# Kernel tuning notes

Hardware: AMD Instinct MI355X
Metric: run time of the kernel (lower is better)

Reference implementation:

```python
import math
import jax, jax.numpy as jnp
import numpy as np

HEAD = 16
D_STATE = 12
DT_RANK = 1


def _ln(x, w, b, eps):
    mu = jnp.mean(x, axis=-1, keepdims=True)
    xc = x - mu
    var = jnp.mean(xc * xc, axis=-1, keepdims=True)
    return xc * jax.lax.rsqrt(var + eps) * w + b


def _chan_ln(x, w, b, eps=1e-6):
    # LayerNorm over channel axis of (B, C, H, W)
    return _ln(x.transpose(0, 2, 3, 1), w, b, eps).transpose(0, 3, 1, 2)


def _gconv1x1(x, w):
    # grouped 1x1 conv; x: (B, Cin, H, W), w: (G, Cout_per_g, Cin_per_g)
    B, Cin, H, W = x.shape
    G, Co, Ci = w.shape
    xg = x.reshape(B, G, Ci, H, W)
    y = jnp.einsum('bgihw,goi->bgohw', xg, w)
    return y.reshape(B, G * Co, H, W)


def _dwconv(x, w, b):
    # depthwise 3x3 conv, SAME padding; w: (C, 1, 3, 3)
    y = jax.lax.conv_general_dilated(x, w, (1, 1), 'SAME',
                                     feature_group_count=x.shape[1])
    return y + b[None, :, None, None]


def setup_inputs() -> dict:
    key = jax.random.key(0)
    ks = jax.random.split(key, 16)
    B, C, H, W = 2, 96, 128, 128
    G, E = 24, 192           # groups = C//4, expand_d = 2*C
    c = E // HEAD            # d_inner per head = 12
    R, N = DT_RANK, D_STATE
    f32 = jnp.float32
    inp = {}
    inp['x_rgb'] = jax.random.normal(ks[0], (B, C, H, W), f32)
    inp['x_e'] = jax.random.normal(ks[1], (B, C, H, W), f32)
    inp['in1_w'] = jnp.ones((C,), f32); inp['in1_b'] = jnp.zeros((C,), f32)
    inp['in2_w'] = jnp.ones((C,), f32); inp['in2_b'] = jnp.zeros((C,), f32)
    inp['inproj_rgb_w'] = jax.random.normal(ks[2], (G, E // G, C // G), f32) * 0.2
    inp['inproj_e_w'] = jax.random.normal(ks[3], (G, E // G, C // G), f32) * 0.2
    inp['conv_rgb_w'] = jax.random.normal(ks[4], (E, 1, 3, 3), f32) * 0.2
    inp['conv_rgb_b'] = jnp.zeros((E,), f32)
    inp['conv_e_w'] = jax.random.normal(ks[5], (E, 1, 3, 3), f32) * 0.2
    inp['conv_e_b'] = jnp.zeros((E,), f32)
    inp['xproj_w'] = jax.random.normal(ks[6], (2, R + 2 * N, HEAD), f32) * (HEAD ** -0.5)
    inp['dtproj_w'] = jax.random.uniform(ks[7], (2, HEAD, R), f32, -R ** -0.5, R ** -0.5)
    dt = jnp.exp(jax.random.uniform(ks[8], (2, HEAD), f32)
                 * (math.log(0.1) - math.log(0.001)) + math.log(0.001))
    dt = jnp.clip(dt, 1e-4, None)
    inp['dtproj_b'] = dt + jnp.log(-jnp.expm1(-dt))  # inverse softplus
    inp['A_logs'] = jnp.log(jnp.broadcast_to(jnp.arange(1, N + 1, dtype=f32), (2, HEAD, N)))
    inp['Ds'] = jnp.ones((2, HEAD), f32)
    inp['on1_w'] = jnp.ones((c,), f32); inp['on1_b'] = jnp.zeros((c,), f32)
    inp['on2_w'] = jnp.ones((c,), f32); inp['on2_b'] = jnp.zeros((c,), f32)
    inp['outproj_rgb_w'] = jax.random.normal(ks[9], (G, C // G, E // G), f32) * 0.2
    inp['outproj_e_w'] = jax.random.normal(ks[10], (G, C // G, E // G), f32) * 0.2
    inp['n1_w'] = jnp.ones((C,), f32); inp['n1_b'] = jnp.zeros((C,), f32)
    inp['n2_w'] = jnp.ones((C,), f32); inp['n2_b'] = jnp.zeros((C,), f32)
    Hd = 4 * C
    inp['mlp_rgb_fc1_w'] = jax.random.normal(ks[11], (Hd, C), f32) * 0.1
    inp['mlp_rgb_fc1_b'] = jnp.zeros((Hd,), f32)
    inp['mlp_rgb_fc2_w'] = jax.random.normal(ks[12], (C, Hd), f32) * 0.05
    inp['mlp_rgb_fc2_b'] = jnp.zeros((C,), f32)
    inp['mlp_e_fc1_w'] = jax.random.normal(ks[13], (Hd, C), f32) * 0.1
    inp['mlp_e_fc1_b'] = jnp.zeros((Hd,), f32)
    inp['mlp_e_fc2_w'] = jax.random.normal(ks[14], (C, Hd), f32) * 0.05
    inp['mlp_e_fc2_b'] = jnp.zeros((C,), f32)
    return inp


def reference(x_rgb, x_e, in1_w, in1_b, in2_w, in2_b, inproj_rgb_w, inproj_e_w,
              conv_rgb_w, conv_rgb_b, conv_e_w, conv_e_b, xproj_w, dtproj_w,
              dtproj_b, A_logs, Ds, on1_w, on1_b, on2_w, on2_b,
              outproj_rgb_w, outproj_e_w, n1_w, n1_b, n2_w, n2_b,
              mlp_rgb_fc1_w, mlp_rgb_fc1_b, mlp_rgb_fc2_w, mlp_rgb_fc2_b,
              mlp_e_fc1_w, mlp_e_fc1_b, mlp_e_fc2_w, mlp_e_fc2_b):
    B, C, H, W = x_rgb.shape
    L = H * W
    R, N = DT_RANK, D_STATE
    # input layer norms (eps=1e-6) over channels
    xr = _chan_ln(x_rgb, in1_w, in1_b)
    xe = _chan_ln(x_e, in2_w, in2_b)
    # grouped 1x1 expand + depthwise conv + SiLU
    ur = jax.nn.silu(_dwconv(_gconv1x1(xr, inproj_rgb_w), conv_rgb_w, conv_rgb_b))
    ue = jax.nn.silu(_dwconv(_gconv1x1(xe, inproj_e_w), conv_e_w, conv_e_b))
    c = ur.shape[1] // HEAD  # d_inner per head

    def to_head(x):  # (B, E, H, W) -> (B, L, head, c)
        return x.transpose(0, 2, 3, 1).reshape(B, L, HEAD, c)

    xs = jnp.stack([to_head(ur), to_head(ue)], axis=2)  # (B, L, 2, head, c)
    # input-dependent dt, B, C projections from the per-head feature (dim=head)
    x_dbl = jnp.einsum('blkdc,krd->blkrc', xs, xproj_w)
    dts = x_dbl[..., :R, :]
    Bs = x_dbl[..., R:R + N, :]          # (B, L, 2, N, c)
    Cs = x_dbl[..., R + N:, :]
    dt = jnp.einsum('blkrc,kdr->blkdc', dts, dtproj_w) + dtproj_b[None, None, :, :, None]
    dt = jax.nn.softplus(dt)             # (B, L, 2, head, c)
    A = -jnp.exp(A_logs)                 # (2, head, N)
    Cs_cross = Cs[:, :, ::-1]            # cross-modal readout: swap modalities
    # selective scan over the channel dim c (sequence axis)
    dt_t = jnp.moveaxis(dt, -1, 0)
    u_t = jnp.moveaxis(xs, -1, 0)
    B_t = jnp.moveaxis(Bs, -1, 0)
    C_t = jnp.moveaxis(Cs_cross, -1, 0)
    h0 = jnp.zeros((B, L, 2, HEAD, N), xs.dtype)

    def step(h, inps):
        dt_s, u_s, B_s, C_s = inps
        dA = jnp.exp(dt_s[..., None] * A)                       # (B,L,2,head,N)
        h = dA * h + (dt_s * u_s)[..., None] * B_s[:, :, :, None, :]
        y = jnp.einsum('blkdn,blkn->blkd', h, C_s)
        return h, y

    _, ys = jax.lax.scan(step, h0, (dt_t, u_t, B_t, C_t))
    y = jnp.moveaxis(ys, 0, -1) + xs * Ds[None, None, :, :, None]  # (B,L,2,head,c)
    # per-head LayerNorm over c (eps=1e-5), back to (B, E, H, W)
    y_r = _ln(y[:, :, 0], on1_w, on1_b, 1e-5).reshape(B, H, W, HEAD * c).transpose(0, 3, 1, 2)
    y_e = _ln(y[:, :, 1], on2_w, on2_b, 1e-5).reshape(B, H, W, HEAD * c).transpose(0, 3, 1, 2)
    y_r = _gconv1x1(y_r, outproj_rgb_w) + xr
    y_e = _gconv1x1(y_e, outproj_e_w) + xe

    def mlp(x, nw, nb, w1, b1, w2, b2):
        z = _chan_ln(x, nw, nb)
        z = jnp.einsum('bchw,oc->bohw', z, w1) + b1[None, :, None, None]
        z = jax.nn.gelu(z, approximate=False)
        z = jnp.einsum('bohw,co->bchw', z, w2) + b2[None, :, None, None]
        return x + z

    y_r = mlp(y_r, n1_w, n1_b, mlp_rgb_fc1_w, mlp_rgb_fc1_b, mlp_rgb_fc2_w, mlp_rgb_fc2_b)
    y_e = mlp(y_e, n2_w, n2_b, mlp_e_fc1_w, mlp_e_fc1_b, mlp_e_fc2_w, mlp_e_fc2_b)
    return (y_r, y_e)
```

## Files before the change

kernel.cpp:

```cpp
#include <hip/hip_runtime.h>
#include <math.h>

#define HWn 16384
#define Hn  128
#define Wn  128
#define Bn  2
#define Cn  96
#define En  192
#define Gn  24
#define HEADn 16
#define CCn 12
#define Nn  12
#define HDn 384

__global__ __launch_bounds__(256) void k_ln_inproj(
    const float* __restrict__ x0, const float* __restrict__ x1,
    const float* __restrict__ lw0, const float* __restrict__ lb0,
    const float* __restrict__ lw1, const float* __restrict__ lb1,
    const float* __restrict__ pw0, const float* __restrict__ pw1,
    float* __restrict__ xr, float* __restrict__ v)
{
  const int s  = blockIdx.y;
  const int gp = blockIdx.x * 256 + threadIdx.x;
  const int b  = gp >> 14, l = gp & (HWn - 1);
  const float* x  = s ? x1  : x0;
  const float* lw = s ? lw1 : lw0;
  const float* lb = s ? lb1 : lb0;
  const float* pw = s ? pw1 : pw0;

  float xv[Cn];
  float sum = 0.f, ss = 0.f;
  const float* xp = x + (size_t)b * Cn * HWn + l;
#pragma unroll
  for (int ch = 0; ch < Cn; ++ch) {
    float t = xp[(size_t)ch * HWn];
    xv[ch] = t; sum += t; ss += t * t;
  }
  float mu  = sum * (1.f / Cn);
  float var = ss * (1.f / Cn) - mu * mu;
  float rs  = rsqrtf(var + 1e-6f);

  float* xrp = xr + ((size_t)s * Bn + b) * Cn * HWn + l;
#pragma unroll
  for (int ch = 0; ch < Cn; ++ch) {
    float n = fmaf((xv[ch] - mu) * rs, lw[ch], lb[ch]);
    xv[ch] = n;
    xrp[(size_t)ch * HWn] = n;
  }

  float* vp = v + ((size_t)s * Bn + b) * En * HWn + l;
#pragma unroll
  for (int g = 0; g < Gn; ++g) {
#pragma unroll
    for (int o = 0; o < 8; ++o) {
      float a = 0.f;
#pragma unroll
      for (int i = 0; i < 4; ++i) a = fmaf(xv[g * 4 + i], pw[g * 32 + o * 4 + i], a);
      vp[(size_t)(g * 8 + o) * HWn] = a;
    }
  }
}

__global__ __launch_bounds__(256) void k_dwconv_silu(
    const float* __restrict__ v,
    const float* __restrict__ cw0, const float* __restrict__ cb0,
    const float* __restrict__ cw1, const float* __restrict__ cb1,
    float* __restrict__ u)
{
  const int z = blockIdx.z;
  const int e = blockIdx.y;
  const int p = blockIdx.x * 256 + threadIdx.x;
  const int h = p >> 7, w = p & 127;
  const int s = z >> 1;
  const float* cw  = (s ? cw1 : cw0) + e * 9;
  const float bias = (s ? cb1 : cb0)[e];
  const float* src = v + ((size_t)z * En + e) * HWn;

  float acc = bias;
#pragma unroll
  for (int kh = 0; kh < 3; ++kh) {
    int hh = h + kh - 1;
    if (hh < 0 || hh >= Hn) continue;
#pragma unroll
    for (int kw = 0; kw < 3; ++kw) {
      int ww = w + kw - 1;
      if (ww < 0 || ww >= Wn) continue;
      acc = fmaf(src[hh * Wn + ww], cw[kh * 3 + kw], acc);
    }
  }
  float sig = 1.f / (1.f + expf(-acc));
  u[((size_t)z * En + e) * HWn + p] = acc * sig;
}

#define UPXS 417
#define USS  208
#define UDS  13
#define XPXS 604
#define XSS  300

__global__ __launch_bounds__(512) void k_ssm(
    const float* __restrict__ u_ws, const float* __restrict__ xr_ws,
    float* __restrict__ z_ws,
    const float* __restrict__ xprojw, const float* __restrict__ dtprojw,
    const float* __restrict__ dtprojb, const float* __restrict__ A_logs,
    const float* __restrict__ Ds,
    const float* __restrict__ on1w, const float* __restrict__ on1b,
    const float* __restrict__ on2w, const float* __restrict__ on2b,
    const float* __restrict__ opw0, const float* __restrict__ opw1)
{
  __shared__ __align__(16) float uS[16 * UPXS];
  __shared__ __align__(16) float xdl[16 * XPXS];

  const int tid  = threadIdx.x;
  const int tile = blockIdx.x;
  const int b  = (tile * 16) >> 14;
  const int l0 = (tile * 16) & (HWn - 1);

  const int p2px = tid >> 5, p2s = (tid >> 4) & 1, p2d = tid & 15;
  const float dtw = dtprojw[p2s * HEADn + p2d];
  const float dtb = dtprojb[p2s * HEADn + p2d];
  const float Dv  = Ds[p2s * HEADn + p2d];
  float Ar[Nn];
  {
    const float4* ap = (const float4*)&A_logs[(p2s * HEADn + p2d) * Nn];
    float4 a0 = ap[0], a1 = ap[1], a2 = ap[2];
    Ar[0]=-expf(a0.x); Ar[1]=-expf(a0.y); Ar[2]=-expf(a0.z); Ar[3]=-expf(a0.w);
    Ar[4]=-expf(a1.x); Ar[5]=-expf(a1.y); Ar[6]=-expf(a1.z); Ar[7]=-expf(a1.w);
    Ar[8]=-expf(a2.x); Ar[9]=-expf(a2.y); Ar[10]=-expf(a2.z); Ar[11]=-expf(a2.w);
  }

#pragma unroll
  for (int i = 0; i < 3; ++i) {
    int id = i * 512 + tid;
    int px4 = id & 3, rest = id >> 2;
    int ch = rest % En, s2 = rest / En;
    float4 t = *(const float4*)&u_ws[(((size_t)s2 * Bn + b) * En + ch) * HWn + l0 + px4 * 4];
    int dd = ch / 12, cc = ch % 12;
    int base = s2 * USS + dd * UDS + cc;
    uS[(px4 * 4 + 0) * UPXS + base] = t.x;
    uS[(px4 * 4 + 1) * UPXS + base] = t.y;
    uS[(px4 * 4 + 2) * UPXS + base] = t.z;
    uS[(px4 * 4 + 3) * UPXS + base] = t.w;
  }
  __syncthreads();

#pragma unroll
  for (int j = 0; j < 2; ++j) {
    int id = j * 512 + tid;
    if (id < 800) {
      int px = id & 15, sr = id >> 4;
      int s2 = sr / 25, r = sr % 25;
      const float4* xw4 = (const float4*)&xprojw[(s2 * 25 + r) * HEADn];
      float4 w0 = xw4[0], w1 = xw4[1], w2 = xw4[2], w3 = xw4[3];
      float wv[16];
      wv[0]=w0.x; wv[1]=w0.y; wv[2]=w0.z; wv[3]=w0.w;
      wv[4]=w1.x; wv[5]=w1.y; wv[6]=w1.z; wv[7]=w1.w;
      wv[8]=w2.x; wv[9]=w2.y; wv[10]=w2.z; wv[11]=w2.w;
      wv[12]=w3.x; wv[13]=w3.y; wv[14]=w3.z; wv[15]=w3.w;
      int ub = px * UPXS + s2 * USS;
      float acc[12];
#pragma unroll
      for (int cc = 0; cc < 12; ++cc) acc[cc] = 0.f;
#pragma unroll
      for (int dd = 0; dd < HEADn; ++dd) {
        float w = wv[dd];
        int ua = ub + dd * UDS;
#pragma unroll
        for (int cc = 0; cc < 12; ++cc)
          acc[cc] = fmaf(uS[ua + cc], w, acc[cc]);
      }
      float* xp = &xdl[px * XPXS + s2 * XSS + r * 12];
      *(float4*)&xp[0] = make_float4(acc[0], acc[1], acc[2], acc[3]);
      *(float4*)&xp[4] = make_float4(acc[4], acc[5], acc[6], acc[7]);
      *(float4*)&xp[8] = make_float4(acc[8], acc[9], acc[10], acc[11]);
    }
  }
  __syncthreads();

  {
    const int px = p2px, s = p2s, d = p2d;
    const int ub = px * UPXS + s * USS + d * UDS;
    float uvv[12];
#pragma unroll
    for (int cc = 0; cc < 12; ++cc) uvv[cc] = uS[ub + cc];

    const int xb = px * XPXS;
    float dts[12];
    {
      const float4* dr = (const float4*)&xdl[xb + s * XSS];
      float4 q0 = dr[0], q1 = dr[1], q2 = dr[2];
      dts[0]=q0.x; dts[1]=q0.y; dts[2]=q0.z; dts[3]=q0.w;
      dts[4]=q1.x; dts[5]=q1.y; dts[6]=q1.z; dts[7]=q1.w;
      dts[8]=q2.x; dts[9]=q2.y; dts[10]=q2.z; dts[11]=q2.w;
    }
    float dt_s[12], dtu[12];
#pragma unroll
    for (int cc = 0; cc < 12; ++cc) {
      float pre = fmaf(dts[cc], dtw, dtb);
      float v = (pre > 20.f) ? pre : log1pf(expf(pre));
      dt_s[cc] = v;
      dtu[cc] = v * uvv[cc];
    }

    float y[12];
#pragma unroll
    for (int cc = 0; cc < 12; ++cc) y[cc] = 0.f;

#pragma unroll
    for (int n = 0; n < Nn; ++n) {
      const float4* Br = (const float4*)&xdl[xb + s * XSS + (1 + n) * 12];
      const float4* Cr = (const float4*)&xdl[xb + (1 - s) * XSS + (13 + n) * 12];
      float4 b0 = Br[0], b1 = Br[1], b2 = Br[2];
      float4 c0 = Cr[0], c1 = Cr[1], c2 = Cr[2];
      float Bv[12], Cv[12];
      Bv[0]=b0.x; Bv[1]=b0.y; Bv[2]=b0.z; Bv[3]=b0.w;
      Bv[4]=b1.x; Bv[5]=b1.y; Bv[6]=b1.z; Bv[7]=b1.w;
      Bv[8]=b2.x; Bv[9]=b2.y; Bv[10]=b2.z; Bv[11]=b2.w;
      Cv[0]=c0.x; Cv[1]=c0.y; Cv[2]=c0.z; Cv[3]=c0.w;
      Cv[4]=c1.x; Cv[5]=c1.y; Cv[6]=c1.z; Cv[7]=c1.w;
      Cv[8]=c2.x; Cv[9]=c2.y; Cv[10]=c2.z; Cv[11]=c2.w;
      float h = 0.f;
      float An = Ar[n];
#pragma unroll
      for (int cc = 0; cc < 12; ++cc) {
        float dA = expf(dt_s[cc] * An);
        h = fmaf(dA, h, dtu[cc] * Bv[cc]);
        y[cc] = fmaf(h, Cv[cc], y[cc]);
      }
    }

#pragma unroll
    for (int cc = 0; cc < 12; ++cc) y[cc] = fmaf(uvv[cc], Dv, y[cc]);

    float mu = 0.f;
#pragma unroll
    for (int cc = 0; cc < 12; ++cc) mu += y[cc];
    mu *= (1.f / CCn);
    float var = 0.f;
#pragma unroll
    for (int cc = 0; cc < 12; ++cc) { float t = y[cc] - mu; var = fmaf(t, t, var); }
    var *= (1.f / CCn);
    float rs = rsqrtf(var + 1e-5f);
    const float* ow = s ? on2w : on1w;
    const float* ob = s ? on2b : on1b;
#pragma unroll
    for (int cc = 0; cc < 12; ++cc)
      uS[ub + cc] = fmaf((y[cc] - mu) * rs, ow[cc], ob[cc]);
  }
  __syncthreads();

#pragma unroll
  for (int i = 0; i < 2; ++i) {
    int id = i * 512 + tid;
    if (id < 768) {
      int px4 = id & 3, ch = (id >> 2) % Cn, ss = id / 384;
      int g = ch >> 2, co = ch & 3;
      const float* ow2 = (ss ? opw1 : opw0) + g * 32 + co * 8;
      float a0 = 0.f, a1 = 0.f, a2 = 0.f, a3 = 0.f;
#pragma unroll
      for (int ci = 0; ci < 8; ++ci) {
        int e = g * 8 + ci;
        int dd = e / 12, cc = e % 12;
        int base = ss * USS + dd * UDS + cc;
        float w = ow2[ci];
        a0 = fmaf(uS[(px4 * 4 + 0) * UPXS + base], w, a0);
        a1 = fmaf(uS[(px4 * 4 + 1) * UPXS + base], w, a1);
        a2 = fmaf(uS[(px4 * 4 + 2) * UPXS + base], w, a2);
        a3 = fmaf(uS[(px4 * 4 + 3) * UPXS + base], w, a3);
      }
      size_t go = (((size_t)ss * Bn + b) * Cn + ch) * HWn + l0 + px4 * 4;
      float4 xrv = *(const float4*)&xr_ws[go];
      *(float4*)&z_ws[go] =
          make_float4(a0 + xrv.x, a1 + xrv.y, a2 + xrv.z, a3 + xrv.w);
    }
  }
}

__global__ void k_transpose_w(
    const float* __restrict__ w1r, const float* __restrict__ w1e,
    const float* __restrict__ w2r, const float* __restrict__ w2e,
    float* __restrict__ w1t, float* __restrict__ w2t)
{
  int idx = blockIdx.x * 256 + threadIdx.x;
  int which = idx / 36864;
  int r = idx % 36864;
  if (which < 2) {
    int c = r / HDn, o = r % HDn;
    const float* src = which ? w1e : w1r;
    w1t[which * 36864 + r] = src[o * Cn + c];
  } else {
    int o = r / Cn, c = r % Cn;
    const float* src = (which == 3) ? w2e : w2r;
    w2t[(which - 2) * 36864 + r] = src[c * HDn + o];
  }
}

__global__ __launch_bounds__(256, 2) void k_mlp(
    const float* __restrict__ z_all,
    const float* __restrict__ n1w, const float* __restrict__ n1b,
    const float* __restrict__ n2w, const float* __restrict__ n2b,
    const float* __restrict__ w1t_all, const float* __restrict__ b1r,
    const float* __restrict__ b1e,
    const float* __restrict__ w2t_all, const float* __restrict__ b2r,
    const float* __restrict__ b2e,
    float* __restrict__ out_all)
{
  __shared__ float zn[Cn * 32];
  __shared__ float hS[HDn * 32];
  __shared__ float red[2 * 8 * 32];
  __shared__ float mus[32], rss[32];

  const int s    = blockIdx.y;
  const int tile = blockIdx.x;
  const int b    = (tile * 32) >> 14;
  const int l0   = (tile * 32) & (HWn - 1);
  const int tid  = threadIdx.x;

  const float* z   = z_all + ((size_t)s * Bn + b) * Cn * HWn + l0;
  float*       out = (float*)out_all + ((size_t)s * Bn + b) * Cn * HWn + l0;
  const float* nw  = s ? n2w : n1w;
  const float* nb  = s ? n2b : n1b;
  const float* w1t = w1t_all + s * 36864;
  const float* b1  = s ? b1e : b1r;
  const float* w2t = w2t_all + s * 36864;
  const float* b2  = s ? b2e : b2r;

  {
    const int px = tid & 31, part = tid >> 5;
    float psum = 0.f, pss = 0.f;
#pragma unroll
    for (int i = 0; i < 12; ++i) {
      int c = part + 8 * i;
      float v = z[(size_t)c * HWn + px];
      zn[c * 32 + px] = v; psum += v; pss += v * v;
    }
    red[part * 32 + px] = psum;
    red[256 + part * 32 + px] = pss;
    __syncthreads();
    if (tid < 32) {
      float sm = 0.f, sq = 0.f;
#pragma unroll
      for (int p = 0; p < 8; ++p) { sm += red[p * 32 + tid]; sq += red[256 + p * 32 + tid]; }
      float mu = sm * (1.f / Cn);
      float var = sq * (1.f / Cn) - mu * mu;
      mus[tid] = mu; rss[tid] = rsqrtf(var + 1e-6f);
    }
    __syncthreads();
    float mu = mus[px], rs = rss[px];
#pragma unroll
    for (int i = 0; i < 12; ++i) {
      int c = part + 8 * i;
      float v = zn[c * 32 + px];
      zn[c * 32 + px] = fmaf((v - mu) * rs, nw[c], nb[c]);
    }
    __syncthreads();
  }

  const int pg = (tid & 7) << 2;

  {
    const int og = (tid >> 3) * 12;
    float acc[12][4];
#pragma unroll
    for (int j = 0; j < 12; ++j)
#pragma unroll
      for (int i = 0; i < 4; ++i) acc[j][i] = 0.f;

    for (int c = 0; c < Cn; ++c) {
      const float* zr = &zn[c * 32 + pg];
      float x0 = zr[0], x1 = zr[1], x2 = zr[2], x3 = zr[3];
      const float* wr = &w1t[c * HDn + og];
#pragma unroll
      for (int j = 0; j < 12; ++j) {
        float w = wr[j];
        acc[j][0] = fmaf(x0, w, acc[j][0]);
        acc[j][1] = fmaf(x1, w, acc[j][1]);
        acc[j][2] = fmaf(x2, w, acc[j][2]);
        acc[j][3] = fmaf(x3, w, acc[j][3]);
      }
    }
#pragma unroll
    for (int j = 0; j < 12; ++j) {
      float bo = b1[og + j];
      float* hr = &hS[(og + j) * 32 + pg];
#pragma unroll
      for (int i = 0; i < 4; ++i) {
        float a = acc[j][i] + bo;
        hr[i] = 0.5f * a * (1.f + erff(a * 0.70710678118654752f));
      }
    }
  }
  __syncthreads();

  {
    const int cg = (tid >> 3) * 3;
    float a0[4], a1[4], a2[4];
#pragma unroll
    for (int i = 0; i < 4; ++i) { a0[i] = 0.f; a1[i] = 0.f; a2[i] = 0.f; }

    for (int o = 0; o < HDn; ++o) {
      const float* hr = &hS[o * 32 + pg];
      float x0 = hr[0], x1 = hr[1], x2 = hr[2], x3 = hr[3];
      const float* wr = &w2t[o * Cn + cg];
      float w0 = wr[0], w1 = wr[1], w2 = wr[2];
      a0[0] = fmaf(x0, w0, a0[0]); a0[1] = fmaf(x1, w0, a0[1]);
      a0[2] = fmaf(x2, w0, a0[2]); a0[3] = fmaf(x3, w0, a0[3]);
      a1[0] = fmaf(x0, w1, a1[0]); a1[1] = fmaf(x1, w1, a1[1]);
      a1[2] = fmaf(x2, w1, a1[2]); a1[3] = fmaf(x3, w1, a1[3]);
      a2[0] = fmaf(x0, w2, a2[0]); a2[1] = fmaf(x1, w2, a2[1]);
      a2[2] = fmaf(x2, w2, a2[2]); a2[3] = fmaf(x3, w2, a2[3]);
    }
#pragma unroll
    for (int k = 0; k < 3; ++k) {
      int c = cg + k;
      float bk = b2[c];
      const float* ak = (k == 0) ? a0 : (k == 1) ? a1 : a2;
#pragma unroll
      for (int i = 0; i < 4; ++i) {
        size_t off = (size_t)c * HWn + pg + i;
        out[off] = ak[i] + bk + z[off];
      }
    }
  }
}

extern "C" void kernel_launch(void* const* d_in, const int* in_sizes, int n_in,
                              void* d_out, int out_size, void* d_ws, size_t ws_size,
                              hipStream_t stream)
{
  const float* x_rgb = (const float*)d_in[0];
  const float* x_e   = (const float*)d_in[1];
  const float* in1_w = (const float*)d_in[2];
  const float* in1_b = (const float*)d_in[3];
  const float* in2_w = (const float*)d_in[4];
  const float* in2_b = (const float*)d_in[5];
  const float* ipw0  = (const float*)d_in[6];
  const float* ipw1  = (const float*)d_in[7];
  const float* cw0   = (const float*)d_in[8];
  const float* cb0   = (const float*)d_in[9];
  const float* cw1   = (const float*)d_in[10];
  const float* cb1   = (const float*)d_in[11];
  const float* xprojw  = (const float*)d_in[12];
  const float* dtprojw = (const float*)d_in[13];
  const float* dtprojb = (const float*)d_in[14];
  const float* A_logs  = (const float*)d_in[15];
  const float* Ds      = (const float*)d_in[16];
  const float* on1w  = (const float*)d_in[17];
  const float* on1b  = (const float*)d_in[18];
  const float* on2w  = (const float*)d_in[19];
  const float* on2b  = (const float*)d_in[20];
  const float* opw0  = (const float*)d_in[21];
  const float* opw1  = (const float*)d_in[22];
  const float* n1w   = (const float*)d_in[23];
  const float* n1b   = (const float*)d_in[24];
  const float* n2w   = (const float*)d_in[25];
  const float* n2b   = (const float*)d_in[26];
  const float* w1r   = (const float*)d_in[27];
  const float* b1r   = (const float*)d_in[28];
  const float* w2r   = (const float*)d_in[29];
  const float* b2r   = (const float*)d_in[30];
  const float* w1e   = (const float*)d_in[31];
  const float* b1e   = (const float*)d_in[32];
  const float* w2e   = (const float*)d_in[33];
  const float* b2e   = (const float*)d_in[34];

  float* ws  = (float*)d_ws;
  float* xr  = ws;
  float* vz  = ws + (size_t)6291456;
  float* ut  = ws + (size_t)18874368;
  float* w1t = ut;
  float* w2t = ut + 73728;

  dim3 b256(256);

  k_ln_inproj<<<dim3(128, 2), b256, 0, stream>>>(
      x_rgb, x_e, in1_w, in1_b, in2_w, in2_b, ipw0, ipw1, xr, vz);

  k_dwconv_silu<<<dim3(64, En, 4), b256, 0, stream>>>(
      vz, cw0, cb0, cw1, cb1, ut);

  k_ssm<<<dim3(2048), dim3(512), 0, stream>>>(
      ut, xr, vz, xprojw, dtprojw, dtprojb, A_logs, Ds,
      on1w, on1b, on2w, on2b, opw0, opw1);

  k_transpose_w<<<dim3(576), b256, 0, stream>>>(w1r, w1e, w2r, w2e, w1t, w2t);

  k_mlp<<<dim3(1024, 2), b256, 0, stream>>>(
      vz, n1w, n1b, n2w, n2b, w1t, b1r, b1e, w2t, b2r, b2e, (float*)d_out);
}
```

Before: 585.9 us.

## Tile LN+in-projection through shared memory and split MLP hidden dim in halves

k_ln_inproj now processes 64-pixel tiles per block, staging the input in shared memory with float4 loads. A block-level reduction computes the LayerNorm statistics, and the grouped projection runs from LDS, replacing one thread per pixel holding 96 registers. The grid grows from 256 to 1024 blocks, which should raise occupancy. k_mlp splits the 384-wide hidden layer into two 192 halves so the hidden-activation shared buffer halves, letting 4 blocks per CU fit, and widens loads to float2/float4 with fewer accumulators per thread. The extra syncs and repeated fc2 accumulation passes add some overhead.

```diff
diff --git a/kernel.cpp b/kernel.cpp
--- a/kernel.cpp
+++ b/kernel.cpp
@@ -13,51 +13,94 @@
 #define Nn  12
 #define HDn 384
 
-__global__ __launch_bounds__(256) void k_ln_inproj(
+#define ZS 68
+
+__global__ __launch_bounds__(256, 4) void k_ln_inproj(
     const float* __restrict__ x0, const float* __restrict__ x1,
     const float* __restrict__ lw0, const float* __restrict__ lb0,
     const float* __restrict__ lw1, const float* __restrict__ lb1,
     const float* __restrict__ pw0, const float* __restrict__ pw1,
     float* __restrict__ xr, float* __restrict__ v)
 {
-  const int s  = blockIdx.y;
-  const int gp = blockIdx.x * 256 + threadIdx.x;
-  const int b  = gp >> 14, l = gp & (HWn - 1);
+  __shared__ __align__(16) float zn[Cn * ZS];
+  __shared__ float red[2 * 16 * 64];
+  __shared__ float mus[64], rss[64];
+
+  const int s    = blockIdx.y;
+  const int tile = blockIdx.x;
+  const int b  = (tile * 64) >> 14;
+  const int l0 = (tile * 64) & (HWn - 1);
+  const int tid = threadIdx.x;
+
   const float* x  = s ? x1  : x0;
   const float* lw = s ? lw1 : lw0;
   const float* lb = s ? lb1 : lb0;
   const float* pw = s ? pw1 : pw0;
 
-  float xv[Cn];
-  float sum = 0.f, ss = 0.f;
-  const float* xp = x + (size_t)b * Cn * HWn + l;
-#pragma unroll
-  for (int ch = 0; ch < Cn; ++ch) {
-    float t = xp[(size_t)ch * HWn];
-    xv[ch] = t; sum += t; ss += t * t;
-  }
-  float mu  = sum * (1.f / Cn);
-  float var = ss * (1.f / Cn) - mu * mu;
-  float rs  = rsqrtf(var + 1e-6f);
-
-  float* xrp = xr + ((size_t)s * Bn + b) * Cn * HWn + l;
-#pragma unroll
-  for (int ch = 0; ch < Cn; ++ch) {
-    float n = fmaf((xv[ch] - mu) * rs, lw[ch], lb[ch]);
-    xv[ch] = n;
-    xrp[(size_t)ch * HWn] = n;
-  }
-
-  float* vp = v + ((size_t)s * Bn + b) * En * HWn + l;
-#pragma unroll
-  for (int g = 0; g < Gn; ++g) {
-#pragma unroll
-    for (int o = 0; o < 8; ++o) {
-      float a = 0.f;
-#pragma unroll
-      for (int i = 0; i < 4; ++i) a = fmaf(xv[g * 4 + i], pw[g * 32 + o * 4 + i], a);
-      vp[(size_t)(g * 8 + o) * HWn] = a;
-    }
+  const int px4 = (tid & 15) * 4;
+  const int cg0 = tid >> 4;
+
+  const float* xp = x + (size_t)b * Cn * HWn + l0;
+  float ps0=0.f,ps1=0.f,ps2=0.f,ps3=0.f, pq0=0.f,pq1=0.f,pq2=0.f,pq3=0.f;
+#pragma unroll
+  for (int i = 0; i < 6; ++i) {
+    int ch = cg0 + 16 * i;
+    float4 t = *(const float4*)&xp[(size_t)ch * HWn + px4];
+    *(float4*)&zn[ch * ZS + px4] = t;
+    ps0 += t.x; pq0 += t.x * t.x;
+    ps1 += t.y; pq1 += t.y * t.y;
+    ps2 += t.z; pq2 += t.z * t.z;
+    ps3 += t.w; pq3 += t.w * t.w;
+  }
+  red[cg0 * 64 + px4 + 0] = ps0; red[1024 + cg0 * 64 + px4 + 0] = pq0;
+  red[cg0 * 64 + px4 + 1] = ps1; red[1024 + cg0 * 64 + px4 + 1] = pq1;
+  red[cg0 * 64 + px4 + 2] = ps2; red[1024 + cg0 * 64 + px4 + 2] = pq2;
+  red[cg0 * 64 + px4 + 3] = ps3; red[1024 + cg0 * 64 + px4 + 3] = pq3;
+  __syncthreads();
+  if (tid < 64) {
+    float sm = 0.f, sq = 0.f;
+#pragma unroll
+    for (int g = 0; g < 16; ++g) { sm += red[g * 64 + tid]; sq += red[1024 + g * 64 + tid]; }
+    float mu = sm * (1.f / Cn);
+    float var = sq * (1.f / Cn) - mu * mu;
+    mus[tid] = mu; rss[tid] = rsqrtf(var + 1e-6f);
+  }
+  __syncthreads();
+
+  const float m0 = mus[px4+0], m1 = mus[px4+1], m2 = mus[px4+2], m3 = mus[px4+3];
+  const float r0 = rss[px4+0], r1 = rss[px4+1], r2 = rss[px4+2], r3 = rss[px4+3];
+  float* xrp = xr + ((size_t)s * Bn + b) * Cn * HWn + l0;
+#pragma unroll
+  for (int i = 0; i < 6; ++i) {
+    int ch = cg0 + 16 * i;
+    float4 t = *(const float4*)&zn[ch * ZS + px4];
+    float wch = lw[ch], bch = lb[ch];
+    t.x = fmaf((t.x - m0) * r0, wch, bch);
+    t.y = fmaf((t.y - m1) * r1, wch, bch);
+    t.z = fmaf((t.z - m2) * r2, wch, bch);
+    t.w = fmaf((t.w - m3) * r3, wch, bch);
+    *(float4*)&zn[ch * ZS + px4] = t;
+    *(float4*)&xrp[(size_t)ch * HWn + px4] = t;
+  }
+  __syncthreads();
+
+  const int og  = (tid >> 4) * 12;
+  const int pxg = (tid & 15) * 4;
+  float* vp = v + ((size_t)s * Bn + b) * En * HWn + l0;
+#pragma unroll
+  for (int jo = 0; jo < 12; ++jo) {
+    int o = og + jo, g = o >> 3;
+    float4 wv = *(const float4*)&pw[g * 32 + (o & 7) * 4];
+    float4 z0 = *(const float4*)&zn[(g * 4 + 0) * ZS + pxg];
+    float4 z1 = *(const float4*)&zn[(g * 4 + 1) * ZS + pxg];
+    float4 z2 = *(const float4*)&zn[(g * 4 + 2) * ZS + pxg];
+    float4 z3 = *(const float4*)&zn[(g * 4 + 3) * ZS + pxg];
+    float4 a;
+    a.x = fmaf(z0.x, wv.x, fmaf(z1.x, wv.y, fmaf(z2.x, wv.z, z3.x * wv.w)));
+    a.y = fmaf(z0.y, wv.x, fmaf(z1.y, wv.y, fmaf(z2.y, wv.z, z3.y * wv.w)));
+    a.z = fmaf(z0.z, wv.x, fmaf(z1.z, wv.y, fmaf(z2.z, wv.z, z3.z * wv.w)));
+    a.w = fmaf(z0.w, wv.x, fmaf(z1.w, wv.y, fmaf(z2.w, wv.z, z3.w * wv.w)));
+    *(float4*)&vp[(size_t)o * HWn + pxg] = a;
   }
 }
 
@@ -295,7 +338,9 @@
   }
 }
 
-__global__ __launch_bounds__(256, 2) void k_mlp(
+#define HSS 34
+
+__global__ __launch_bounds__(256, 4) void k_mlp(
     const float* __restrict__ z_all,
     const float* __restrict__ n1w, const float* __restrict__ n1b,
     const float* __restrict__ n2w, const float* __restrict__ n2b,
@@ -306,7 +351,7 @@
     float* __restrict__ out_all)
 {
   __shared__ float zn[Cn * 32];
-  __shared__ float hS[HDn * 32];
+  __shared__ float hS[192 * HSS];
   __shared__ float red[2 * 8 * 32];
   __shared__ float mus[32], rss[32];
 
@@ -356,71 +401,78 @@
     __syncthreads();
   }
 
-  const int pg = (tid & 7) << 2;
-
-  {
-    const int og = (tid >> 3) * 12;
-    float acc[12][4];
-#pragma unroll
-    for (int j = 0; j < 12; ++j)
+  const int pg   = (tid & 7) << 2;
+  const int og   = (tid >> 3) * 6;
+  const int p2px = (tid & 15) * 2;
+  const int cg   = (tid >> 4) * 6;
+
+  float a2[6][2];
+#pragma unroll
+  for (int k = 0; k < 6; ++k) { a2[k][0] = 0.f; a2[k][1] = 0.f; }
+
+#pragma unroll
+  for (int hf = 0; hf < 2; ++hf) {
+    float acc[6][4];
+#pragma unroll
+    for (int j = 0; j < 6; ++j)
 #pragma unroll
       for (int i = 0; i < 4; ++i) acc[j][i] = 0.f;
 
+    const float* w1base = w1t + hf * 192 + og;
     for (int c = 0; c < Cn; ++c) {
-      const float* zr = &zn[c * 32 + pg];
-      float x0 = zr[0], x1 = zr[1], x2 = zr[2], x3 = zr[3];
-      const float* wr = &w1t[c * HDn + og];
-#pragma unroll
-      for (int j = 0; j < 12; ++j) {
-        float w = wr[j];
-        acc[j][0] = fmaf(x0, w, acc[j][0]);
-        acc[j][1] = fmaf(x1, w, acc[j][1]);
-        acc[j][2] = fmaf(x2, w, acc[j][2]);
-        acc[j][3] = fmaf(x3, w, acc[j][3]);
+      float4 xv = *(const float4*)&zn[c * 32 + pg];
+      const float* wr = w1base + c * HDn;
+      float2 wa = *(const float2*)&wr[0];
+      float2 wb = *(const float2*)&wr[2];
+      float2 wc = *(const float2*)&wr[4];
+      float w[6] = {wa.x, wa.y, wb.x, wb.y, wc.x, wc.y};
+#pragma unroll
+      for (int j = 0; j < 6; ++j) {
+        acc[j][0] = fmaf(xv.x, w[j], acc[j][0]);
+        acc[j][1] = fmaf(xv.y, w[j], acc[j][1]);
+        acc[j][2] = fmaf(xv.z, w[j], acc[j][2]);
+        acc[j][3] = fmaf(xv.w, w[j], acc[j][3]);
       }
     }
 #pragma unroll
-    for (int j = 0; j < 12; ++j) {
-      float bo = b1[og + j];
-      float* hr = &hS[(og + j) * 32 + pg];
-#pragma unroll
-      for (int i = 0; i < 4; ++i) {
-        float a = acc[j][i] + bo;
-        hr[i] = 0.5f * a * (1.f + erff(a * 0.70710678118654752f));
-      }
-    }
-  }
-  __syncthreads();
-
-  {
-    const int cg = (tid >> 3) * 3;
-    float a0[4], a1[4], a2[4];
-#pragma unroll
-    for (int i = 0; i < 4; ++i) { a0[i] = 0.f; a1[i] = 0.f; a2[i] = 0.f; }
-
-    for (int o = 0; o < HDn; ++o) {
-      const float* hr = &hS[o * 32 + pg];
-      float x0 = hr[0], x1 = hr[1], x2 = hr[2], x3 = hr[3];
-      const float* wr = &w2t[o * Cn + cg];
-      float w0 = wr[0], w1 = wr[1], w2 = wr[2];
-      a0[0] = fmaf(x0, w0, a0[0]); a0[1] = fmaf(x1, w0, a0[1]);
-      a0[2] = fmaf(x2, w0, a0[2]); a0[3] = fmaf(x3, w0, a0[3]);
-      a1[0] = fmaf(x0, w1, a1[0]); a1[1] = fmaf(x1, w1, a1[1]);
-      a1[2] = fmaf(x2, w1, a1[2]); a1[3] = fmaf(x3, w1, a1[3]);
-      a2[0] = fmaf(x0, w2, a2[0]); a2[1] = fmaf(x1, w2, a2[1]);
-      a2[2] = fmaf(x2, w2, a2[2]); a2[3] = fmaf(x3, w2, a2[3]);
-    }
-#pragma unroll
-    for (int k = 0; k < 3; ++k) {
-      int c = cg + k;
-      float bk = b2[c];
-      const float* ak = (k == 0) ? a0 : (k == 1) ? a1 : a2;
-#pragma unroll
-      for (int i = 0; i < 4; ++i) {
-        size_t off = (size_t)c * HWn + pg + i;
-        out[off] = ak[i] + bk + z[off];
-      }
-    }
+    for (int j = 0; j < 6; ++j) {
+      float bo = b1[hf * 192 + og + j];
+      float g0 = acc[j][0] + bo, g1 = acc[j][1] + bo;
+      float g2 = acc[j][2] + bo, g3 = acc[j][3] + bo;
+      g0 = 0.5f * g0 * (1.f + erff(g0 * 0.70710678118654752f));
+      g1 = 0.5f * g1 * (1.f + erff(g1 * 0.70710678118654752f));
+      g2 = 0.5f * g2 * (1.f + erff(g2 * 0.70710678118654752f));
+      g3 = 0.5f * g3 * (1.f + erff(g3 * 0.70710678118654752f));
+      float* hr = &hS[(og + j) * HSS + pg];
+      *(float2*)&hr[0] = make_float2(g0, g1);
+      *(float2*)&hr[2] = make_float2(g2, g3);
+    }
+    __syncthreads();
+
+    const float* w2base = w2t + (hf * 192) * Cn + cg;
+    for (int o = 0; o < 192; ++o) {
+      float2 hv = *(const float2*)&hS[o * HSS + p2px];
+      const float* wr = w2base + o * Cn;
+      float2 wa = *(const float2*)&wr[0];
+      float2 wb = *(const float2*)&wr[2];
+      float2 wc = *(const float2*)&wr[4];
+      a2[0][0] = fmaf(hv.x, wa.x, a2[0][0]); a2[0][1] = fmaf(hv.y, wa.x, a2[0][1]);
+      a2[1][0] = fmaf(hv.x, wa.y, a2[1][0]); a2[1][1] = fmaf(hv.y, wa.y, a2[1][1]);
+      a2[2][0] = fmaf(hv.x, wb.x, a2[2][0]); a2[2][1] = fmaf(hv.y, wb.x, a2[2][1]);
+      a2[3][0] = fmaf(hv.x, wb.y, a2[3][0]); a2[3][1] = fmaf(hv.y, wb.y, a2[3][1]);
+      a2[4][0] = fmaf(hv.x, wc.x, a2[4][0]); a2[4][1] = fmaf(hv.y, wc.x, a2[4][1]);
+      a2[5][0] = fmaf(hv.x, wc.y, a2[5][0]); a2[5][1] = fmaf(hv.y, wc.y, a2[5][1]);
+    }
+    __syncthreads();
+  }
+
+#pragma unroll
+  for (int k = 0; k < 6; ++k) {
+    int c = cg + k;
+    float bk = b2[c];
+    size_t off = (size_t)c * HWn + p2px;
+    float2 zv = *(const float2*)&z[off];
+    *(float2*)&out[off] = make_float2(a2[k][0] + bk + zv.x, a2[k][1] + bk + zv.y);
   }
 }
 
@@ -473,7 +525,7 @@
 
   dim3 b256(256);
 
-  k_ln_inproj<<<dim3(128, 2), b256, 0, stream>>>(
+  k_ln_inproj<<<dim3(512, 2), b256, 0, stream>>>(
       x_rgb, x_e, in1_w, in1_b, in2_w, in2_b, ipw0, ipw1, xr, vz);
 
   k_dwconv_silu<<<dim3(64, En, 4), b256, 0, stream>>>(
```

New measurement: 669.3 us. 14.2% more time.
